# Performance work log

Hardware: AMD Instinct MI355X
Metric: run time of the kernel (lower is better)

The kernel has to match this reference:

```python
import jax, jax.numpy as jnp
import numpy as np

EPS = 1e-8

def _mlp(z, W1, b1, W2, b2):
    # Two Blocks (Linear + ReLU), widths per n_layers=[512,128]
    z = jax.nn.relu(z @ W1 + b1)
    z = jax.nn.relu(z @ W2 + b2)
    return z

def setup_inputs() -> dict:
    key = jax.random.key(0)
    ks = jax.random.split(key, 5)
    B, N, D = 1024, 30000, 256
    H1, H2 = 512, 128
    x = jax.random.normal(ks[0], (B, D), dtype=jnp.float32)
    sub_x = jax.random.normal(ks[1], (N, D), dtype=jnp.float32)
    sub_y = jax.random.uniform(ks[2], (N,), dtype=jnp.float32)
    W1 = jax.random.normal(ks[3], (D, H1), dtype=jnp.float32) * (1.0 / np.sqrt(D))
    b1 = jnp.zeros((H1,), dtype=jnp.float32)
    W2 = jax.random.normal(ks[4], (H1, H2), dtype=jnp.float32) * (1.0 / np.sqrt(H1))
    b2 = jnp.zeros((H2,), dtype=jnp.float32)
    return {"x": x, "sub_x": sub_x, "sub_y": sub_y, "W1": W1, "b1": b1, "W2": W2, "b2": b2}

def reference(x, sub_x, sub_y, W1, b1, W2, b2):
    h = _mlp(x, W1, b1, W2, b2)          # [B, d]
    sh = _mlp(sub_x, W1, b1, W2, b2)     # [N, d]
    # Pairwise squared euclidean via ||a||^2 + ||b||^2 - 2 a.b (GEMM form,
    # same math as the broadcasted diff-and-reduce in the torch code)
    x2 = jnp.sum(h * h, axis=-1, keepdims=True)        # [B, 1]
    s2 = jnp.sum(sh * sh, axis=-1)[None, :]            # [1, N]
    d2 = jnp.maximum(x2 + s2 - 2.0 * (h @ sh.T), 0.0)  # [B, N]
    dist = jnp.sqrt(d2 + EPS)
    alpha = jax.nn.softmax(-dist, axis=-1)             # [B, N]
    return alpha @ sub_y                               # [B]
```

## Files before the change

kernel.cpp:

```cpp
#include <hip/hip_runtime.h>
#include <hip/hip_bf16.h>
#include <math.h>

#define EPSF 1e-8f

typedef __attribute__((ext_vector_type(8))) short bf16x8;
typedef __attribute__((ext_vector_type(4))) float f32x4;

static __device__ __forceinline__ unsigned short f2bf(float f) {
    __hip_bfloat16 h = __float2bfloat16(f);
    return *reinterpret_cast<unsigned short*>(&h);
}
static __device__ __forceinline__ float bf2f(unsigned short u) {
    __hip_bfloat16 h;
    *reinterpret_cast<unsigned short*>(&h) = u;
    return __bfloat162float(h);
}

static __device__ __forceinline__ void async16(void* lds, const void* g) {
    __builtin_amdgcn_global_load_lds(
        (const __attribute__((address_space(1))) unsigned int*)g,
        (__attribute__((address_space(3))) unsigned int*)lds, 16, 0, 0);
}


__global__ __launch_bounds__(256) void prep(
    const float* __restrict__ subx, const float* __restrict__ x,
    const float* __restrict__ W1, const float* __restrict__ W2,
    unsigned short* __restrict__ XF,
    unsigned short* __restrict__ w1h, unsigned short* __restrict__ w2h,
    float* __restrict__ gl, float* __restrict__ gy, float* __restrict__ nrm,
    int M, int nsubrow, int nsplitblk)
{
    __shared__ __align__(16) unsigned short sX[8192];
    const int t = threadIdx.x;
    const int b = blockIdx.x;

    if (b < nsplitblk) {
        int gi = b * 256 + t;
        float4 z = make_float4(0.f, 0.f, 0.f, 0.f);
        if (gi < 512) {
            if (gi < 256) ((float4*)gl)[gi] = z;
            else          ((float4*)gy)[gi - 256] = z;
        }
        if (gi < (M + 3) / 4) ((float4*)nrm)[gi] = z;

        const int rbase = b * 32;
        const int rows = min(32, M - rbase);
        #pragma unroll
        for (int it = 0; it < 8; ++it) {
            int flat = it * 256 + t;
            int row = flat >> 6;
            int k = (flat & 63) * 4;
            if (row < rows) {
                int grow = rbase + row;
                const float* src = (grow < nsubrow)
                    ? subx + (size_t)grow * 256 + k
                    : x + (size_t)(grow - nsubrow) * 256 + k;
                float4 v = *(const float4*)src;
                unsigned short h0 = f2bf(v.x), h1 = f2bf(v.y), h2 = f2bf(v.z), h3 = f2bf(v.w);
                uint2 hp;
                hp.x = ((unsigned)h1 << 16) | h0;  hp.y = ((unsigned)h3 << 16) | h2;
                int chunk = (row >> 4) * 8 + (k >> 5);
                int lne = (row & 15) | (((k >> 3) & 3) << 4);
                *(uint2*)&sX[chunk * 512 + lne * 8 + (k & 7)] = hp;
            }
        }
        __syncthreads();
        const int cvalid = (rows >> 4) * 8;
        const size_t base = (size_t)rbase * 256;
        #pragma unroll
        for (int it = 0; it < 4; ++it) {
            int flat = it * 256 + t;
            if ((flat >> 6) < cvalid)
                *(bf16x8*)&XF[base + flat * 8] = *(const bf16x8*)&sX[flat * 8];
        }
    } else if (b < nsplitblk + 512) {
        int idx = (b - nsplitblk) * 256 + t;
        int n = idx >> 8, k = idx & 255;
        float w = W1[(size_t)k * 512 + n];
        int chunk = (n >> 4) * 8 + (k >> 5);
        int lne = (n & 15) | (((k >> 3) & 3) << 4);
        w1h[chunk * 512 + lne * 8 + (k & 7)] = f2bf(w);
    } else {
        int idx = (b - nsplitblk - 512) * 256 + t;
        int n = idx >> 9, k = idx & 511;
        float w = W2[(size_t)k * 128 + n];
        int chunk = (n >> 4) * 16 + (k >> 5);
        int lne = (n & 15) | (((k >> 3) & 3) << 4);
        w2h[chunk * 512 + lne * 8 + (k & 7)] = f2bf(w);
    }
}

__global__ __launch_bounds__(256) void gemm_l1(
    const unsigned short* __restrict__ XF,
    const unsigned short* __restrict__ BhF,
    const float* __restrict__ bias, unsigned short* __restrict__ z1F, int M)
{
    __shared__ __align__(16) unsigned short sB[16384];

    const int nb = gridDim.x;
    const int per = nb >> 3, rem = nb & 7;
    const int xcd = blockIdx.x & 7, slot = blockIdx.x >> 3;
    const int newbid = xcd * per + min(xcd, rem) + slot;
    const int m0 = (newbid >> 3) * 128, n0 = (newbid & 7) * 64;

    const int t = threadIdx.x, wave = t >> 6, lane = t & 63;
    const int quad = lane >> 4, lq = lane & 15;
    const int lastch = (M >> 4) - 1;

    #pragma unroll
    for (int q = 0; q < 8; ++q) {
        int c = wave * 8 + q;
        int nc = c >> 3, kc = c & 7;
        const unsigned short* src = BhF
            + ((size_t)((n0 >> 4) + nc)) * 4096 + kc * 512 + lane * 8;
        async16(sB + c * 512, src);
    }

    const unsigned short* pA[2];
    #pragma unroll
    for (int mi = 0; mi < 2; ++mi) {
        int mc = min((m0 >> 4) + wave * 2 + mi, lastch);
        pA[mi] = XF + (size_t)mc * 4096 + lane * 8;
    }

    f32x4 acc[2][4];
    #pragma unroll
    for (int i = 0; i < 2; ++i)
        #pragma unroll
        for (int j = 0; j < 4; ++j) acc[i][j] = (f32x4){0.f, 0.f, 0.f, 0.f};

    __syncthreads();

    #pragma unroll
    for (int kc = 0; kc < 8; ++kc) {
        bf16x8 fA[2];
        #pragma unroll
        for (int mi = 0; mi < 2; ++mi)
            fA[mi] = *(const bf16x8*)(pA[mi] + kc * 512);
        #pragma unroll
        for (int ni = 0; ni < 4; ++ni) {
            bf16x8 fB = *(const bf16x8*)&sB[(ni * 8 + kc) * 512 + lane * 8];
            #pragma unroll
            for (int mi = 0; mi < 2; ++mi)
                acc[mi][ni] = __builtin_amdgcn_mfma_f32_16x16x32_bf16(fA[mi], fB, acc[mi][ni], 0, 0, 0);
        }
    }

    __syncthreads();
    unsigned short* ctile = sB;
    float bv[4];
    #pragma unroll
    for (int ni = 0; ni < 4; ++ni) bv[ni] = bias[n0 + ni * 16 + lq];
    #pragma unroll
    for (int mi = 0; mi < 2; ++mi)
        #pragma unroll
        for (int ni = 0; ni < 4; ++ni)
            #pragma unroll
            for (int r = 0; r < 4; ++r) {
                float v = fmaxf(acc[mi][ni][r] + bv[ni], 0.f);
                ctile[(wave * 32 + mi * 16 + quad * 4 + r) * 72 + ni * 16 + lq] = f2bf(v);
            }
    __syncthreads();
    #pragma unroll
    for (int it = 0; it < 4; ++it) {
        int flat = it * 256 + t;
        int c = flat >> 6, l = flat & 63;
        int mcl = c >> 1, kc2 = c & 1;
        int gmc = (m0 >> 4) + mcl;
        if (gmc * 16 < M) {
            bf16x8 v = *(const bf16x8*)&ctile[(mcl * 16 + (l & 15)) * 72 + kc2 * 32 + (l >> 4) * 8];
            *(bf16x8*)&z1F[((size_t)gmc * 16 + (n0 >> 5) + kc2) * 512 + l * 8] = v;
        }
    }
}

__global__ __launch_bounds__(256) void gemm_l2_norm(
    const unsigned short* __restrict__ AF,
    const unsigned short* __restrict__ BhF,
    const float* __restrict__ bias, unsigned short* __restrict__ embF,
    float* __restrict__ nrm, int M)
{
    __shared__ __align__(16) unsigned short sB[18432];

    const int nb = gridDim.x;
    const int per = nb >> 3, rem = nb & 7;
    const int xcd = blockIdx.x & 7, slot = blockIdx.x >> 3;
    const int newbid = xcd * per + min(xcd, rem) + slot;
    const int m0 = (newbid >> 2) * 256, n0 = (newbid & 3) * 32;

    const int t = threadIdx.x, wave = t >> 6, lane = t & 63;
    const int quad = lane >> 4, lq = lane & 15;
    const int lastch = (M >> 4) - 1;

    #pragma unroll
    for (int q = 0; q < 8; ++q) {
        int c = wave * 8 + q;
        int nc = c >> 4, kc = c & 15;
        const unsigned short* src = BhF
            + ((size_t)((n0 >> 4) + nc)) * 8192 + kc * 512 + lane * 8;
        async16(sB + c * 512, src);
    }

    const unsigned short* pA[4];
    #pragma unroll
    for (int mi = 0; mi < 4; ++mi) {
        int mc = min((m0 >> 4) + wave * 4 + mi, lastch);
        pA[mi] = AF + (size_t)mc * 8192 + lane * 8;
    }

    f32x4 acc[4][2];
    #pragma unroll
    for (int i = 0; i < 4; ++i)
        #pragma unroll
        for (int j = 0; j < 2; ++j) acc[i][j] = (f32x4){0.f, 0.f, 0.f, 0.f};

    __syncthreads();

    #pragma unroll 4
    for (int kc = 0; kc < 16; ++kc) {
        bf16x8 fA[4];
        #pragma unroll
        for (int mi = 0; mi < 4; ++mi)
            fA[mi] = *(const bf16x8*)(pA[mi] + kc * 512);
        #pragma unroll
        for (int ni = 0; ni < 2; ++ni) {
            bf16x8 fB = *(const bf16x8*)&sB[(ni * 16 + kc) * 512 + lane * 8];
            #pragma unroll
            for (int mi = 0; mi < 4; ++mi)
                acc[mi][ni] = __builtin_amdgcn_mfma_f32_16x16x32_bf16(fA[mi], fB, acc[mi][ni], 0, 0, 0);
        }
    }

    __syncthreads();
    unsigned short* ctile = sB;
    float bv[2];
    #pragma unroll
    for (int ni = 0; ni < 2; ++ni) bv[ni] = bias[n0 + ni * 16 + lq];
    #pragma unroll
    for (int mi = 0; mi < 4; ++mi)
        #pragma unroll
        for (int ni = 0; ni < 2; ++ni)
            #pragma unroll
            for (int r = 0; r < 4; ++r) {
                float v = fmaxf(acc[mi][ni][r] + bv[ni], 0.f);
                ctile[(wave * 64 + mi * 16 + quad * 4 + r) * 36 + ni * 16 + lq] = f2bf(v);
            }
    __syncthreads();

    #pragma unroll
    for (int it = 0; it < 4; ++it) {
        int flat = it * 256 + t;
        int c = flat >> 6, l = flat & 63;
        int gmc = (m0 >> 4) + c;
        if (gmc * 16 < M) {
            bf16x8 v = *(const bf16x8*)&ctile[(c * 16 + (l & 15)) * 36 + (l >> 4) * 8];
            *(bf16x8*)&embF[((size_t)gmc * 4 + (n0 >> 5)) * 512 + l * 8] = v;
        }
    }
    int gm = m0 + t;
    if (gm < M) {
        float s = 0.f;
        #pragma unroll
        for (int seg = 0; seg < 4; ++seg) {
            bf16x8 v = *(const bf16x8*)&ctile[t * 36 + seg * 8];
            #pragma unroll
            for (int e = 0; e < 8; ++e) {
                float f = bf2f((unsigned short)v[e]);
                s = fmaf(f, f, s);
            }
        }
        atomicAdd(&nrm[gm], s);
    }
}

__global__ __launch_bounds__(256) void nca_flash_mfma(
    const unsigned short* __restrict__ embF, const float* __restrict__ nrm,
    const float* __restrict__ y, float* __restrict__ gl, float* __restrict__ gy,
    int N, int jspan)
{
    __shared__ __align__(16) unsigned short sB[16384];
    __shared__ float s2s[128], ys[128];

    const int t = threadIdx.x, wave = t >> 6, lane = t & 63;
    const int quad = lane >> 4, lq = lane & 15;
    const int i0 = blockIdx.x * 64;
    const int j0base = blockIdx.y * jspan;
    const int jend = min(j0base + jspan, N);

    bf16x8 fa[4];
    const int hc = ((N + i0) >> 4) + wave;
    #pragma unroll
    for (int kk = 0; kk < 4; ++kk)
        fa[kk] = *(const bf16x8*)&embF[((size_t)hc * 4 + kk) * 512 + lane * 8];
    float myh2[4];
    #pragma unroll
    for (int r = 0; r < 4; ++r) myh2[r] = nrm[N + i0 + wave * 16 + quad * 4 + r];

    float lacc[4] = {0.f, 0.f, 0.f, 0.f};
    float yacc[4] = {0.f, 0.f, 0.f, 0.f};

    for (int j0 = j0base; j0 < jend; j0 += 128) {
        __syncthreads();
        #pragma unroll
        for (int q = 0; q < 8; ++q) {
            int c = wave * 8 + q;
            async16(sB + c * 512,
                    embF + ((size_t)(j0 >> 4) * 4 + c) * 512 + lane * 8);
        }
        if (t < 128) {
            int j = j0 + t;
            s2s[t] = (j < jend) ? nrm[j] : 1e30f;
            ys[t]  = (j < jend) ? y[j] : 0.f;
        }
        __syncthreads();

        f32x4 acc[8];
        #pragma unroll
        for (int jt = 0; jt < 8; ++jt) acc[jt] = (f32x4){0.f, 0.f, 0.f, 0.f};
        #pragma unroll
        for (int kk = 0; kk < 4; ++kk) {
            #pragma unroll
            for (int jt = 0; jt < 8; ++jt) {
                bf16x8 b = *(const bf16x8*)&sB[(jt * 4 + kk) * 512 + lane * 8];
                acc[jt] = __builtin_amdgcn_mfma_f32_16x16x32_bf16(fa[kk], b, acc[jt], 0, 0, 0);
            }
        }

        #pragma unroll
        for (int jt = 0; jt < 8; ++jt) {
            int col = jt * 16 + lq;
            float ss = s2s[col];
            float sy = ys[col];
            #pragma unroll
            for (int r = 0; r < 4; ++r) {
                float d2 = myh2[r] + ss - 2.f * acc[jt][r];
                float d  = sqrtf(fmaxf(d2, 0.f) + EPSF);
                float p  = __expf(-d);
                lacc[r] += p;
                yacc[r]  = fmaf(p, sy, yacc[r]);
            }
        }
    }

    #pragma unroll
    for (int r = 0; r < 4; ++r) {
        #pragma unroll
        for (int off = 8; off > 0; off >>= 1) {
            lacc[r] += __shfl_down(lacc[r], off, 16);
            yacc[r] += __shfl_down(yacc[r], off, 16);
        }
    }
    if (lq == 0) {
        int row = i0 + wave * 16 + quad * 4;
        #pragma unroll
        for (int r = 0; r < 4; ++r) {
            atomicAdd(&gl[row + r], lacc[r]);
            atomicAdd(&gy[row + r], yacc[r]);
        }
    }
}

__global__ __launch_bounds__(256) void finalize_div(
    const float* __restrict__ gl, const float* __restrict__ gy,
    float* __restrict__ out, int B)
{
    int i = blockIdx.x * 256 + threadIdx.x;
    if (i < B) out[i] = gy[i] / gl[i];
}

extern "C" void kernel_launch(void* const* d_in, const int* in_sizes, int n_in,
                              void* d_out, int out_size, void* d_ws, size_t ws_size,
                              hipStream_t stream)
{
    const float* x    = (const float*)d_in[0];
    const float* subx = (const float*)d_in[1];
    const float* suby = (const float*)d_in[2];
    const float* W1   = (const float*)d_in[3];
    const float* b1   = (const float*)d_in[4];
    const float* W2   = (const float*)d_in[5];
    const float* b2   = (const float*)d_in[6];
    float* out = (float*)d_out;

    const int B = 1024, N = 30000, D = 256, H1 = 512, H2 = 128;
    const int M = N + B;

    char* wsb = (char*)d_ws;
    size_t off = 0;
    auto alloc = [&](size_t bytes) -> char* {
        char* p = wsb + off;
        off += (bytes + 255) & ~(size_t)255;
        return p;
    };
    unsigned short* cx   = (unsigned short*)alloc((size_t)M * D * 2);
    unsigned short* w1hT = (unsigned short*)alloc((size_t)H1 * D * 2);
    unsigned short* w2hT = (unsigned short*)alloc((size_t)H2 * H1 * 2);
    unsigned short* z1   = (unsigned short*)alloc((size_t)M * H1 * 2);
    unsigned short* emb  = (unsigned short*)alloc((size_t)M * H2 * 2);
    float* nrm = (float*)alloc((size_t)M * 4);
    float* gl  = (float*)alloc((size_t)B * 4);
    float* gy  = (float*)alloc((size_t)B * 4);
    (void)ws_size; (void)in_sizes; (void)n_in; (void)out_size;

    dim3 blk(256);
    const int NSPLITBLK = (M + 31) / 32;
    prep<<<dim3(NSPLITBLK + 512 + 256), blk, 0, stream>>>(
        subx, x, W1, W2, cx, w1hT, w2hT, gl, gy, nrm, M, N, NSPLITBLK);
    gemm_l1<<<dim3(((M + 127) / 128) * (H1 / 64)), blk, 0, stream>>>(
        cx, w1hT, b1, z1, M);
    gemm_l2_norm<<<dim3(((M + 255) / 256) * (H2 / 32)), blk, 0, stream>>>(
        z1, w2hT, b2, emb, nrm, M);
    const int JSPAN = 512;
    const int NSPLIT = (N + JSPAN - 1) / JSPAN;
    nca_flash_mfma<<<dim3(B / 64, NSPLIT), blk, 0, stream>>>(
        emb, nrm, suby, gl, gy, N, JSPAN);
    finalize_div<<<dim3(B / 256), blk, 0, stream>>>(gl, gy, out, B);
}
```

Baseline: 149.1 us.

## Fuse both MLP layers into one kernel keeping hidden activations in LDS

Adds a fused MLP kernel in which each block takes 64 rows, computes layer 1 against W1 chunks streamed through double-buffered LDS, and writes the ReLU output as bf16 into swizzled LDS. Layer 2 then consumes that tile directly and emits the embeddings and row norms. This removes the global write and re-read of the M x 512 intermediate and one kernel launch. The cost is 128KB of dynamic LDS per block, which limits occupancy, and every block restreams all of W1 and W2. The old two-kernel path remains as a fallback if the shared-memory attribute cannot be set.

```diff
diff --git a/kernel.cpp b/kernel.cpp
--- a/kernel.cpp
+++ b/kernel.cpp
@@ -92,6 +92,168 @@
     }
 }
 
+static __device__ __forceinline__ void stage_chunk(
+    unsigned short* dst, const unsigned short* w1f, const unsigned short* w2f,
+    int s, int wave, int lane)
+{
+    #pragma unroll
+    for (int q = 0; q < 8; ++q) {
+        int fl = wave * 8 + q;
+        const unsigned short* src;
+        if (s < 8) src = w1f + (size_t)s * 16384 + fl * 512;
+        else       src = w2f + ((size_t)((fl & 7) * 16 + (s - 8) * 4 + (fl >> 3))) * 512;
+        async16(dst + fl * 512, src + lane * 8);
+    }
+}
+
+__global__ __launch_bounds__(256) void mlp_fused(
+    const unsigned short* __restrict__ XF,
+    const unsigned short* __restrict__ W1F,
+    const unsigned short* __restrict__ W2F,
+    const float* __restrict__ b1, const float* __restrict__ b2,
+    unsigned short* __restrict__ embF, float* __restrict__ nrm, int M)
+{
+    extern __shared__ __align__(16) char smem[];
+    unsigned short* buf0 = (unsigned short*)(smem + 65536);
+    unsigned short* buf1 = (unsigned short*)(smem + 65536 + 32768);
+
+    const int t = threadIdx.x, wave = t >> 6, lane = t & 63;
+    const int quad = lane >> 4, lq = lane & 15;
+    const int m0 = blockIdx.x * 64;
+    const int lastch = (M >> 4) - 1;
+
+    const int mh = wave >> 1, np = wave & 1;
+
+    bf16x8 fA[2][8];
+    #pragma unroll
+    for (int mi = 0; mi < 2; ++mi) {
+        int gmc = min((m0 >> 4) + mh * 2 + mi, lastch);
+        #pragma unroll
+        for (int kc = 0; kc < 8; ++kc)
+            fA[mi][kc] = *(const bf16x8*)&XF[(size_t)gmc * 4096 + kc * 512 + lane * 8];
+    }
+    float b1v[16];
+    #pragma unroll
+    for (int i = 0; i < 16; ++i)
+        b1v[i] = b1[(i >> 1) * 64 + (np * 2 + (i & 1)) * 16 + lq];
+    float b2v[8];
+    #pragma unroll
+    for (int i = 0; i < 8; ++i) b2v[i] = b2[i * 16 + lq];
+
+    f32x4 acc2[8];
+    #pragma unroll
+    for (int i = 0; i < 8; ++i) acc2[i] = (f32x4){0.f, 0.f, 0.f, 0.f};
+
+    __syncthreads();
+
+    stage_chunk(buf0, W1F, W2F, 0, wave, lane);
+    #pragma unroll
+    for (int c = 0; c < 12; ++c) {
+        if (c < 11) {
+            stage_chunk(((c + 1) & 1) ? buf1 : buf0, W1F, W2F, c + 1, wave, lane);
+            asm volatile("s_waitcnt vmcnt(8)" ::: "memory");
+        } else {
+            asm volatile("s_waitcnt vmcnt(0)" ::: "memory");
+        }
+        __builtin_amdgcn_s_barrier();
+        const unsigned short* sW = (c & 1) ? buf1 : buf0;
+
+        if (c < 8) {
+            f32x4 a1[2][2];
+            #pragma unroll
+            for (int mi = 0; mi < 2; ++mi)
+                #pragma unroll
+                for (int nl = 0; nl < 2; ++nl) a1[mi][nl] = (f32x4){0.f, 0.f, 0.f, 0.f};
+            __builtin_amdgcn_s_setprio(1);
+            #pragma unroll
+            for (int kc = 0; kc < 8; ++kc) {
+                #pragma unroll
+                for (int nl = 0; nl < 2; ++nl) {
+                    bf16x8 fB = *(const bf16x8*)&sW[((np * 2 + nl) * 8 + kc) * 512 + lane * 8];
+                    #pragma unroll
+                    for (int mi = 0; mi < 2; ++mi)
+                        a1[mi][nl] = __builtin_amdgcn_mfma_f32_16x16x32_bf16(
+                            fA[mi][kc], fB, a1[mi][nl], 0, 0, 0);
+                }
+            }
+            __builtin_amdgcn_s_setprio(0);
+            #pragma unroll
+            for (int mi = 0; mi < 2; ++mi) {
+                #pragma unroll
+                for (int nl = 0; nl < 2; ++nl) {
+                    int col = c * 64 + (np * 2 + nl) * 16 + lq;
+                    #pragma unroll
+                    for (int r = 0; r < 4; ++r) {
+                        int row = (mh * 2 + mi) * 16 + quad * 4 + r;
+                        float v = fmaxf(a1[mi][nl][r] + b1v[c * 2 + nl], 0.f);
+                        int off = (row * 1024 + col * 2) ^ ((row & 7) << 4);
+                        *(unsigned short*)(smem + off) = f2bf(v);
+                    }
+                }
+            }
+        } else {
+            const int Q = c - 8;
+            const int row = wave * 16 + lq;
+            const int sw = (row & 7) << 4;
+            __builtin_amdgcn_s_setprio(1);
+            #pragma unroll
+            for (int gs = 0; gs < 4; ++gs) {
+                int k2c = Q * 4 + gs;
+                int offa = (row * 1024 + (k2c * 32 + quad * 8) * 2) ^ sw;
+                bf16x8 a2 = *(const bf16x8*)(smem + offa);
+                #pragma unroll
+                for (int nc = 0; nc < 8; ++nc) {
+                    bf16x8 fB = *(const bf16x8*)&sW[(gs * 8 + nc) * 512 + lane * 8];
+                    acc2[nc] = __builtin_amdgcn_mfma_f32_16x16x32_bf16(a2, fB, acc2[nc], 0, 0, 0);
+                }
+            }
+            __builtin_amdgcn_s_setprio(0);
+        }
+        asm volatile("s_waitcnt lgkmcnt(0)" ::: "memory");
+        __builtin_amdgcn_s_barrier();
+    }
+
+    __syncthreads();
+    unsigned short* ct = (unsigned short*)smem;
+    #pragma unroll
+    for (int nc = 0; nc < 8; ++nc) {
+        #pragma unroll
+        for (int r = 0; r < 4; ++r) {
+            int row = wave * 16 + quad * 4 + r;
+            float v = fmaxf(acc2[nc][r] + b2v[nc], 0.f);
+            ct[row * 136 + nc * 16 + lq] = f2bf(v);
+        }
+    }
+    __syncthreads();
+    #pragma unroll
+    for (int it = 0; it < 4; ++it) {
+        int flat = it * 256 + t;
+        int lc = flat >> 6, l = flat & 63;
+        int mcl = lc >> 2, kc = lc & 3;
+        int gmc2 = (m0 >> 4) + mcl;
+        if (gmc2 * 16 < M) {
+            bf16x8 v = *(const bf16x8*)&ct[(mcl * 16 + (l & 15)) * 136 + kc * 32 + (l >> 4) * 8];
+            *(bf16x8*)&embF[((size_t)gmc2 * 4 + kc) * 512 + l * 8] = v;
+        }
+    }
+    if (t < 64) {
+        int gm = m0 + t;
+        if (gm < M) {
+            float s = 0.f;
+            #pragma unroll
+            for (int seg = 0; seg < 16; ++seg) {
+                bf16x8 v = *(const bf16x8*)&ct[t * 136 + seg * 8];
+                #pragma unroll
+                for (int e = 0; e < 8; ++e) {
+                    float f = bf2f((unsigned short)v[e]);
+                    s = fmaf(f, f, s);
+                }
+            }
+            nrm[gm] = s;
+        }
+    }
+}
+
 __global__ __launch_bounds__(256) void gemm_l1(
     const unsigned short* __restrict__ XF,
     const unsigned short* __restrict__ BhF,
@@ -369,6 +531,8 @@
     int i = blockIdx.x * 256 + threadIdx.x;
     if (i < B) out[i] = gy[i] / gl[i];
 }
+
+static int g_fused_ok = -1;
 
 extern "C" void kernel_launch(void* const* d_in, const int* in_sizes, int n_in,
                               void* d_out, int out_size, void* d_ws, size_t ws_size,
@@ -403,14 +567,27 @@
     float* gy  = (float*)alloc((size_t)B * 4);
     (void)ws_size; (void)in_sizes; (void)n_in; (void)out_size;
 
+    if (g_fused_ok < 0) {
+        hipError_t e = hipFuncSetAttribute((const void*)mlp_fused,
+            hipFuncAttributeMaxDynamicSharedMemorySize, 131072);
+        g_fused_ok = (e == hipSuccess) ? 1 : 0;
+    }
+
     dim3 blk(256);
     const int NSPLITBLK = (M + 31) / 32;
     prep<<<dim3(NSPLITBLK + 512 + 256), blk, 0, stream>>>(
         subx, x, W1, W2, cx, w1hT, w2hT, gl, gy, nrm, M, N, NSPLITBLK);
-    gemm_l1<<<dim3(((M + 127) / 128) * (H1 / 64)), blk, 0, stream>>>(
-        cx, w1hT, b1, z1, M);
-    gemm_l2_norm<<<dim3(((M + 255) / 256) * (H2 / 32)), blk, 0, stream>>>(
-        z1, w2hT, b2, emb, nrm, M);
+
+    if (g_fused_ok) {
+        mlp_fused<<<dim3((M + 63) / 64), blk, 131072, stream>>>(
+            cx, w1hT, w2hT, b1, b2, emb, nrm, M);
+    } else {
+        gemm_l1<<<dim3(((M + 127) / 128) * (H1 / 64)), blk, 0, stream>>>(
+            cx, w1hT, b1, z1, M);
+        gemm_l2_norm<<<dim3(((M + 255) / 256) * (H2 / 32)), blk, 0, stream>>>(
+            z1, w2hT, b2, emb, nrm, M);
+    }
+
     const int JSPAN = 512;
     const int NSPLIT = (N + JSPAN - 1) / JSPAN;
     nca_flash_mfma<<<dim3(B / 64, NSPLIT), blk, 0, stream>>>(
```

Measured after the change: 150.7 us. About the same (+1.0%).
